# Performance work log

Hardware: AMD Instinct MI355X
Metric: run time of the kernel (lower is better)

## Reference

```python
import jax, jax.numpy as jnp
import numpy as np

I_DIM = 20000        # item (node) count; emb_mat has I_DIM+1 rows
EMB_DIM = 128        # input embedding dim
D_DIM = 128          # hidden (scaled) dim
N_EDGES = 640000     # number of (src, dst) edges


def setup_inputs() -> dict:
    key = jax.random.key(0)
    k1, k2, k3, k4 = jax.random.split(key, 4)
    emb_mat = jax.random.normal(k1, (I_DIM + 1, EMB_DIM), dtype=jnp.float32)
    # edges must be sorted by source node (column 0) so that the original
    # tf.repeat(segment_sums, bincount(src)) trick is well-defined.
    edge = jax.random.randint(k2, (N_EDGES, 2), 0, I_DIM + 1, dtype=jnp.int64)
    order = jnp.argsort(edge[:, 0])
    edge = edge[order]
    W_scale = jax.random.normal(k3, (EMB_DIM, D_DIM), dtype=jnp.float32) * 0.05
    b_scale = jnp.zeros((D_DIM,), dtype=jnp.float32)
    W_att = jax.random.normal(k4, (2 * D_DIM, 1), dtype=jnp.float32) * 0.05
    b_att = jnp.zeros((1,), dtype=jnp.float32)
    return {"emb_mat": emb_mat, "edge": edge, "W_scale": W_scale,
            "b_scale": b_scale, "W_att": W_att, "b_att": b_att}


def reference(emb_mat, edge, W_scale, b_scale, W_att, b_att):
    num_segments = emb_mat.shape[0]          # i_dim + 1
    seg = edge[:, 0]                         # source nodes (segment ids), [E]

    # gather both endpoints, scale: [E, 2, emb] -> [E, 2, d]
    edge_emb = emb_mat[edge] @ W_scale + b_scale
    E = edge_emb.shape[0]
    # attention logit per edge from concatenated endpoint features
    att = (edge_emb.reshape(E, -1) @ W_att + b_att)[:, 0]   # [E]
    att = jax.nn.leaky_relu(att, negative_slope=0.2)
    scores = jnp.exp(att - 1.0)                              # exp(att - ones)

    # manual segment softmax over edges grouped by source node
    score_sum = jax.ops.segment_sum(scores, seg, num_segments=num_segments)
    score_norm = scores / score_sum[seg]                     # [E]

    # scale all node embeddings once, gather destination features
    item_scaled = emb_mat @ W_scale + b_scale                # [N, d]
    items = item_scaled[edge[:, 1]]                          # [E, d]

    agg = jax.ops.segment_sum(score_norm[:, None] * items, seg,
                              num_segments=num_segments)     # [N, d]
    return jax.nn.sigmoid(agg)
```

## Files before the change

### kernel.cpp

```cpp
#include <hip/hip_runtime.h>
#include <math.h>

#define NSEG 20001
#define EMB  128
#define NE   640000

#define SCALE_BLOCKS ((NSEG + 15) / 16)
#define BOUNDS_BLOCKS ((NE + 255) / 256)

__device__ __forceinline__ float dot4(float4 a, float4 b) {
    return a.x*b.x + a.y*b.y + a.z*b.z + a.w*b.w;
}

#define FMA4(acc, s, b) { acc.x += (s)*(b).x; acc.y += (s)*(b).y; acc.z += (s)*(b).z; acc.w += (s)*(b).w; }

__device__ __forceinline__ unsigned short f2bf(float x) {
    unsigned u = __float_as_uint(x);
    unsigned r = (u + 0x7fffu + ((u >> 16) & 1u)) >> 16;
    return (unsigned short)r;
}

__global__ __launch_bounds__(256) void prep_kernel(
    const float* __restrict__ emb, const float* __restrict__ W,
    const float* __restrict__ bsc, const float* __restrict__ Watt,
    const int* __restrict__ edge,
    unsigned short* __restrict__ tab,
    float* __restrict__ a_src, float* __restrict__ a_dst,
    int* __restrict__ seg_start)
{
    const int tid = threadIdx.x;
    if (blockIdx.x >= SCALE_BLOCKS) {
        int e = (blockIdx.x - SCALE_BLOCKS) * 256 + tid;
        if (e >= NE) return;
        int s  = edge[2*e];
        int sp = (e == 0) ? -1 : edge[2*e - 2];
        for (int t = sp + 1; t <= s; ++t) seg_start[t] = e;
        if (e == NE - 1) {
            for (int t = s + 1; t <= NSEG; ++t) seg_start[t] = NE;
        }
        return;
    }

    __shared__ float emb_s[16 * EMB];
    const int r0 = blockIdx.x * 16;

    const float4* embg4 = (const float4*)emb;
    float4* es4 = (float4*)emb_s;
    const int gmax = NSEG * 32 - 1;
    #pragma unroll
    for (int j = 0; j < 2; ++j) {
        int idx = tid + j * 256;
        int g = r0 * 32 + idx;
        es4[idx] = embg4[g <= gmax ? g : gmax];
    }
    __syncthreads();

    const int cg = tid & 31;
    const int rb = (tid >> 5) * 2;

    float4 acc0 = {0.f,0.f,0.f,0.f};
    float4 acc1 = {0.f,0.f,0.f,0.f};
    const float4* Wg4 = (const float4*)W;

    for (int k = 0; k < EMB; k += 4) {
        float4 b0 = Wg4[(k+0)*32 + cg];
        float4 b1 = Wg4[(k+1)*32 + cg];
        float4 b2 = Wg4[(k+2)*32 + cg];
        float4 b3 = Wg4[(k+3)*32 + cg];
        float4 a0 = *(const float4*)&emb_s[(rb+0)*EMB + k];
        float4 a1 = *(const float4*)&emb_s[(rb+1)*EMB + k];
        FMA4(acc0, a0.x, b0); FMA4(acc0, a0.y, b1); FMA4(acc0, a0.z, b2); FMA4(acc0, a0.w, b3);
        FMA4(acc1, a1.x, b0); FMA4(acc1, a1.y, b1); FMA4(acc1, a1.z, b2); FMA4(acc1, a1.w, b3);
    }

    float4 bs = *(const float4*)&bsc[cg*4];
    acc0.x += bs.x; acc0.y += bs.y; acc0.z += bs.z; acc0.w += bs.w;
    acc1.x += bs.x; acc1.y += bs.y; acc1.z += bs.z; acc1.w += bs.w;

    const int row0 = r0 + rb;
    const int row1 = row0 + 1;
    if (row0 < NSEG) {
        ushort4 p = { f2bf(acc0.x), f2bf(acc0.y), f2bf(acc0.z), f2bf(acc0.w) };
        *(ushort4*)&tab[row0*EMB + cg*4] = p;
    }
    if (row1 < NSEG) {
        ushort4 p = { f2bf(acc1.x), f2bf(acc1.y), f2bf(acc1.z), f2bf(acc1.w) };
        *(ushort4*)&tab[row1*EMB + cg*4] = p;
    }

    float4 ws = *(const float4*)&Watt[cg*4];
    float4 wd = *(const float4*)&Watt[EMB + cg*4];
    float p0s = dot4(acc0, ws), p0d = dot4(acc0, wd);
    float p1s = dot4(acc1, ws), p1d = dot4(acc1, wd);
    #pragma unroll
    for (int off = 16; off >= 1; off >>= 1) {
        p0s += __shfl_xor(p0s, off);
        p0d += __shfl_xor(p0d, off);
        p1s += __shfl_xor(p1s, off);
        p1d += __shfl_xor(p1d, off);
    }
    if ((tid & 31) == 0) {
        if (row0 < NSEG) { a_src[row0] = p0s; a_dst[row0] = p0d; }
        if (row1 < NSEG) { a_src[row1] = p1s; a_dst[row1] = p1d; }
    }
}

__device__ __forceinline__ float bcastf(float v, int j) {
    return __uint_as_float(__builtin_amdgcn_readlane(__float_as_uint(v), j));
}
__device__ __forceinline__ float bf_lo(unsigned u) { return __uint_as_float(u << 16); }
__device__ __forceinline__ float bf_hi(unsigned u) { return __uint_as_float(u & 0xffff0000u); }

__global__ __launch_bounds__(256) void agg_kernel(
    const int* __restrict__ edge, const float* __restrict__ a_src,
    const float* __restrict__ a_dst, const float* __restrict__ b_att,
    const int* __restrict__ seg_start, const unsigned int* __restrict__ tab32,
    float* __restrict__ out)
{
    const int wid = blockIdx.x * 4 + (threadIdx.x >> 6);
    if (wid >= NSEG) return;
    const int lane = threadIdx.x & 63;
    const unsigned int* tabl = tab32 + lane;

    const int s0 = seg_start[wid];
    const int s1 = seg_start[wid + 1];
    const float aS = a_src[wid] + b_att[0];

    float accx = 0.f, accy = 0.f, ssum = 0.f;

    for (int cb = s0; cb < s1; cb += 64) {
        int n = s1 - cb; if (n > 64) n = 64;
        int e = cb + lane;
        int dmine = 0; float sc = 0.f;
        if (lane < n) {
            dmine = edge[2*e + 1] << 6;
            float att = aS + a_dst[dmine >> 6];
            att = att > 0.f ? att : 0.2f * att;
            sc  = expf(att - 1.f);
        }
        ssum += sc;

        int j = 0;
        for (; j + 3 < n; j += 4) {
            float w0 = bcastf(sc, j+0), w1 = bcastf(sc, j+1);
            float w2 = bcastf(sc, j+2), w3 = bcastf(sc, j+3);
            int d0 = __builtin_amdgcn_readlane(dmine, j+0);
            int d1 = __builtin_amdgcn_readlane(dmine, j+1);
            int d2 = __builtin_amdgcn_readlane(dmine, j+2);
            int d3 = __builtin_amdgcn_readlane(dmine, j+3);
            unsigned u0 = tabl[d0];
            unsigned u1 = tabl[d1];
            unsigned u2 = tabl[d2];
            unsigned u3 = tabl[d3];
            accx += w0 * bf_lo(u0); accy += w0 * bf_hi(u0);
            accx += w1 * bf_lo(u1); accy += w1 * bf_hi(u1);
            accx += w2 * bf_lo(u2); accy += w2 * bf_hi(u2);
            accx += w3 * bf_lo(u3); accy += w3 * bf_hi(u3);
        }
        for (; j < n; ++j) {
            float w = bcastf(sc, j);
            int   d = __builtin_amdgcn_readlane(dmine, j);
            unsigned u = tabl[d];
            accx += w * bf_lo(u);
            accy += w * bf_hi(u);
        }
    }

    #pragma unroll
    for (int off = 32; off >= 1; off >>= 1) ssum += __shfl_xor(ssum, off);

    const float inv = (s1 > s0) ? 1.f / ssum : 0.f;
    float ox = accx * inv, oy = accy * inv;
    ox = 1.f / (1.f + expf(-ox));
    oy = 1.f / (1.f + expf(-oy));
    *(float2*)&out[wid * EMB + 2 * lane] = make_float2(ox, oy);
}

extern "C" void kernel_launch(void* const* d_in, const int* in_sizes, int n_in,
                              void* d_out, int out_size, void* d_ws, size_t ws_size,
                              hipStream_t stream) {
    const float* emb  = (const float*)d_in[0];
    const int*   edge = (const int*)  d_in[1];
    const float* W    = (const float*)d_in[2];
    const float* bsc  = (const float*)d_in[3];
    const float* Watt = (const float*)d_in[4];
    const float* batt = (const float*)d_in[5];
    float* out = (float*)d_out;

    unsigned short* tab = (unsigned short*)d_ws;
    float* a_src = (float*)(tab + (size_t)NSEG * EMB);
    float* a_dst = a_src + NSEG;
    int*   seg_start = (int*)(a_dst + NSEG);

    prep_kernel<<<SCALE_BLOCKS + BOUNDS_BLOCKS, 256, 0, stream>>>(
        emb, W, bsc, Watt, edge, tab, a_src, a_dst, seg_start);
    agg_kernel<<<(NSEG + 3) / 4, 256, 0, stream>>>(
        edge, a_src, a_dst, batt, seg_start, (const unsigned int*)tab, out);
}
```

Measured before the change: 116.1 us.

## Retile scale GEMM to 64 rows per block and compact destination indices

The prep GEMM now processes 64 rows per block with a padded LDS stride, and each thread computes a 4x8 register tile, reusing W loads across more rows. The bounds pass reads edges as int2, uses a wave shuffle for the previous source id, and writes a compact dst array so the aggregation kernel reads 4 bytes per edge instead of strided pairs. The aggregation inner loop is unrolled to 8 gathers in flight. It costs more registers and LDS per block and an extra workspace write of the destination array.

Result: faster. 111.4 us (-4.1%).

```diff
diff --git a/kernel.cpp b/kernel.cpp
--- a/kernel.cpp
+++ b/kernel.cpp
@@ -5,8 +5,9 @@
 #define EMB  128
 #define NE   640000
 
-#define SCALE_BLOCKS ((NSEG + 15) / 16)
-#define BOUNDS_BLOCKS ((NE + 255) / 256)
+#define SCALE_BLOCKS 313
+#define BOUNDS_BLOCKS 2500
+#define LDSL 129
 
 __device__ __forceinline__ float dot4(float4 a, float4 b) {
     return a.x*b.x + a.y*b.y + a.z*b.z + a.w*b.w;
@@ -14,10 +15,9 @@
 
 #define FMA4(acc, s, b) { acc.x += (s)*(b).x; acc.y += (s)*(b).y; acc.z += (s)*(b).z; acc.w += (s)*(b).w; }
 
-__device__ __forceinline__ unsigned short f2bf(float x) {
+__device__ __forceinline__ unsigned f2bf(float x) {
     unsigned u = __float_as_uint(x);
-    unsigned r = (u + 0x7fffu + ((u >> 16) & 1u)) >> 16;
-    return (unsigned short)r;
+    return (u + 0x7fffu + ((u >> 16) & 1u)) >> 16;
 }
 
 __global__ __launch_bounds__(256) void prep_kernel(
@@ -26,93 +26,101 @@
     const int* __restrict__ edge,
     unsigned short* __restrict__ tab,
     float* __restrict__ a_src, float* __restrict__ a_dst,
-    int* __restrict__ seg_start)
+    int* __restrict__ seg_start, int* __restrict__ dst)
 {
     const int tid = threadIdx.x;
     if (blockIdx.x >= SCALE_BLOCKS) {
         int e = (blockIdx.x - SCALE_BLOCKS) * 256 + tid;
-        if (e >= NE) return;
-        int s  = edge[2*e];
-        int sp = (e == 0) ? -1 : edge[2*e - 2];
-        for (int t = sp + 1; t <= s; ++t) seg_start[t] = e;
+        int2 p = ((const int2*)edge)[e];
+        dst[e] = p.y;
+        int sp = __shfl_up(p.x, 1);
+        if ((tid & 63) == 0) sp = (e == 0) ? -1 : edge[2*e - 2];
+        for (int t = sp + 1; t <= p.x; ++t) seg_start[t] = e;
         if (e == NE - 1) {
-            for (int t = s + 1; t <= NSEG; ++t) seg_start[t] = NE;
+            for (int t = p.x + 1; t <= NSEG; ++t) seg_start[t] = NE;
         }
         return;
     }
 
-    __shared__ float emb_s[16 * EMB];
-    const int r0 = blockIdx.x * 16;
+    __shared__ float emb_s[64 * LDSL];
+    const int r0 = blockIdx.x * 64;
 
     const float4* embg4 = (const float4*)emb;
-    float4* es4 = (float4*)emb_s;
     const int gmax = NSEG * 32 - 1;
     #pragma unroll
-    for (int j = 0; j < 2; ++j) {
+    for (int j = 0; j < 8; ++j) {
         int idx = tid + j * 256;
+        int row = idx >> 5, f4 = idx & 31;
         int g = r0 * 32 + idx;
-        es4[idx] = embg4[g <= gmax ? g : gmax];
+        float4 v = embg4[g <= gmax ? g : gmax];
+        float* p = &emb_s[row * LDSL + f4 * 4];
+        p[0] = v.x; p[1] = v.y; p[2] = v.z; p[3] = v.w;
     }
     __syncthreads();
 
-    const int cg = tid & 31;
-    const int rb = (tid >> 5) * 2;
-
-    float4 acc0 = {0.f,0.f,0.f,0.f};
-    float4 acc1 = {0.f,0.f,0.f,0.f};
+    const int cg   = tid & 15;
+    const int rowb = (tid >> 4) * 4;
+
+    float4 accA[4] = {{0,0,0,0},{0,0,0,0},{0,0,0,0},{0,0,0,0}};
+    float4 accB[4] = {{0,0,0,0},{0,0,0,0},{0,0,0,0},{0,0,0,0}};
     const float4* Wg4 = (const float4*)W;
 
-    for (int k = 0; k < EMB; k += 4) {
-        float4 b0 = Wg4[(k+0)*32 + cg];
-        float4 b1 = Wg4[(k+1)*32 + cg];
-        float4 b2 = Wg4[(k+2)*32 + cg];
-        float4 b3 = Wg4[(k+3)*32 + cg];
-        float4 a0 = *(const float4*)&emb_s[(rb+0)*EMB + k];
-        float4 a1 = *(const float4*)&emb_s[(rb+1)*EMB + k];
-        FMA4(acc0, a0.x, b0); FMA4(acc0, a0.y, b1); FMA4(acc0, a0.z, b2); FMA4(acc0, a0.w, b3);
-        FMA4(acc1, a1.x, b0); FMA4(acc1, a1.y, b1); FMA4(acc1, a1.z, b2); FMA4(acc1, a1.w, b3);
-    }
-
-    float4 bs = *(const float4*)&bsc[cg*4];
-    acc0.x += bs.x; acc0.y += bs.y; acc0.z += bs.z; acc0.w += bs.w;
-    acc1.x += bs.x; acc1.y += bs.y; acc1.z += bs.z; acc1.w += bs.w;
-
-    const int row0 = r0 + rb;
-    const int row1 = row0 + 1;
-    if (row0 < NSEG) {
-        ushort4 p = { f2bf(acc0.x), f2bf(acc0.y), f2bf(acc0.z), f2bf(acc0.w) };
-        *(ushort4*)&tab[row0*EMB + cg*4] = p;
-    }
-    if (row1 < NSEG) {
-        ushort4 p = { f2bf(acc1.x), f2bf(acc1.y), f2bf(acc1.z), f2bf(acc1.w) };
-        *(ushort4*)&tab[row1*EMB + cg*4] = p;
-    }
-
-    float4 ws = *(const float4*)&Watt[cg*4];
-    float4 wd = *(const float4*)&Watt[EMB + cg*4];
-    float p0s = dot4(acc0, ws), p0d = dot4(acc0, wd);
-    float p1s = dot4(acc1, ws), p1d = dot4(acc1, wd);
+    #pragma unroll 4
+    for (int k = 0; k < EMB; ++k) {
+        float4 w0 = Wg4[k*32 + cg*2];
+        float4 w1 = Wg4[k*32 + cg*2 + 1];
+        float a0 = emb_s[(rowb+0)*LDSL + k];
+        float a1 = emb_s[(rowb+1)*LDSL + k];
+        float a2 = emb_s[(rowb+2)*LDSL + k];
+        float a3 = emb_s[(rowb+3)*LDSL + k];
+        FMA4(accA[0], a0, w0); FMA4(accB[0], a0, w1);
+        FMA4(accA[1], a1, w0); FMA4(accB[1], a1, w1);
+        FMA4(accA[2], a2, w0); FMA4(accB[2], a2, w1);
+        FMA4(accA[3], a3, w0); FMA4(accB[3], a3, w1);
+    }
+
+    const float4 bsA = *(const float4*)&bsc[cg*8];
+    const float4 bsB = *(const float4*)&bsc[cg*8 + 4];
+    const float4 wsA = *(const float4*)&Watt[cg*8];
+    const float4 wsB = *(const float4*)&Watt[cg*8 + 4];
+    const float4 wdA = *(const float4*)&Watt[EMB + cg*8];
+    const float4 wdB = *(const float4*)&Watt[EMB + cg*8 + 4];
+
     #pragma unroll
-    for (int off = 16; off >= 1; off >>= 1) {
-        p0s += __shfl_xor(p0s, off);
-        p0d += __shfl_xor(p0d, off);
-        p1s += __shfl_xor(p1s, off);
-        p1d += __shfl_xor(p1d, off);
-    }
-    if ((tid & 31) == 0) {
-        if (row0 < NSEG) { a_src[row0] = p0s; a_dst[row0] = p0d; }
-        if (row1 < NSEG) { a_src[row1] = p1s; a_dst[row1] = p1d; }
-    }
-}
-
+    for (int r = 0; r < 4; ++r) {
+        float4 A = accA[r], B = accB[r];
+        A.x += bsA.x; A.y += bsA.y; A.z += bsA.z; A.w += bsA.w;
+        B.x += bsB.x; B.y += bsB.y; B.z += bsB.z; B.w += bsB.w;
+        const int row = r0 + rowb + r;
+
+        if (row < NSEG) {
+            uint4 pkt;
+            pkt.x = f2bf(A.x) | (f2bf(A.y) << 16);
+            pkt.y = f2bf(A.z) | (f2bf(A.w) << 16);
+            pkt.z = f2bf(B.x) | (f2bf(B.y) << 16);
+            pkt.w = f2bf(B.z) | (f2bf(B.w) << 16);
+            ((uint4*)tab)[row * 16 + cg] = pkt;
+        }
+
+        float ps = dot4(A, wsA) + dot4(B, wsB);
+        float pd = dot4(A, wdA) + dot4(B, wdB);
+        #pragma unroll
+        for (int off = 8; off >= 1; off >>= 1) {
+            ps += __shfl_xor(ps, off);
+            pd += __shfl_xor(pd, off);
+        }
+        if (cg == 0 && row < NSEG) { a_src[row] = ps; a_dst[row] = pd; }
+    }
+}
+
+__device__ __forceinline__ float bf_lo(unsigned u) { return __uint_as_float(u << 16); }
+__device__ __forceinline__ float bf_hi(unsigned u) { return __uint_as_float(u & 0xffff0000u); }
 __device__ __forceinline__ float bcastf(float v, int j) {
     return __uint_as_float(__builtin_amdgcn_readlane(__float_as_uint(v), j));
 }
-__device__ __forceinline__ float bf_lo(unsigned u) { return __uint_as_float(u << 16); }
-__device__ __forceinline__ float bf_hi(unsigned u) { return __uint_as_float(u & 0xffff0000u); }
 
 __global__ __launch_bounds__(256) void agg_kernel(
-    const int* __restrict__ edge, const float* __restrict__ a_src,
+    const int* __restrict__ dst, const float* __restrict__ a_src,
     const float* __restrict__ a_dst, const float* __restrict__ b_att,
     const int* __restrict__ seg_start, const unsigned int* __restrict__ tab32,
     float* __restrict__ out)
@@ -133,7 +141,7 @@
         int e = cb + lane;
         int dmine = 0; float sc = 0.f;
         if (lane < n) {
-            dmine = edge[2*e + 1] << 6;
+            dmine = dst[e] << 6;
             float att = aS + a_dst[dmine >> 6];
             att = att > 0.f ? att : 0.2f * att;
             sc  = expf(att - 1.f);
@@ -141,21 +149,29 @@
         ssum += sc;
 
         int j = 0;
-        for (; j + 3 < n; j += 4) {
+        for (; j + 7 < n; j += 8) {
             float w0 = bcastf(sc, j+0), w1 = bcastf(sc, j+1);
             float w2 = bcastf(sc, j+2), w3 = bcastf(sc, j+3);
+            float w4 = bcastf(sc, j+4), w5 = bcastf(sc, j+5);
+            float w6 = bcastf(sc, j+6), w7 = bcastf(sc, j+7);
             int d0 = __builtin_amdgcn_readlane(dmine, j+0);
             int d1 = __builtin_amdgcn_readlane(dmine, j+1);
             int d2 = __builtin_amdgcn_readlane(dmine, j+2);
             int d3 = __builtin_amdgcn_readlane(dmine, j+3);
-            unsigned u0 = tabl[d0];
-            unsigned u1 = tabl[d1];
-            unsigned u2 = tabl[d2];
-            unsigned u3 = tabl[d3];
+            int d4 = __builtin_amdgcn_readlane(dmine, j+4);
+            int d5 = __builtin_amdgcn_readlane(dmine, j+5);
+            int d6 = __builtin_amdgcn_readlane(dmine, j+6);
+            int d7 = __builtin_amdgcn_readlane(dmine, j+7);
+            unsigned u0 = tabl[d0], u1 = tabl[d1], u2 = tabl[d2], u3 = tabl[d3];
+            unsigned u4 = tabl[d4], u5 = tabl[d5], u6 = tabl[d6], u7 = tabl[d7];
             accx += w0 * bf_lo(u0); accy += w0 * bf_hi(u0);
             accx += w1 * bf_lo(u1); accy += w1 * bf_hi(u1);
             accx += w2 * bf_lo(u2); accy += w2 * bf_hi(u2);
             accx += w3 * bf_lo(u3); accy += w3 * bf_hi(u3);
+            accx += w4 * bf_lo(u4); accy += w4 * bf_hi(u4);
+            accx += w5 * bf_lo(u5); accy += w5 * bf_hi(u5);
+            accx += w6 * bf_lo(u6); accy += w6 * bf_hi(u6);
+            accx += w7 * bf_lo(u7); accy += w7 * bf_hi(u7);
         }
         for (; j < n; ++j) {
             float w = bcastf(sc, j);
@@ -191,9 +207,10 @@
     float* a_src = (float*)(tab + (size_t)NSEG * EMB);
     float* a_dst = a_src + NSEG;
     int*   seg_start = (int*)(a_dst + NSEG);
+    int*   dstc = seg_start + NSEG + 3;
 
     prep_kernel<<<SCALE_BLOCKS + BOUNDS_BLOCKS, 256, 0, stream>>>(
-        emb, W, bsc, Watt, edge, tab, a_src, a_dst, seg_start);
+        emb, W, bsc, Watt, edge, tab, a_src, a_dst, seg_start, dstc);
     agg_kernel<<<(NSEG + 3) / 4, 256, 0, stream>>>(
-        edge, a_src, a_dst, batt, seg_start, (const unsigned int*)tab, out);
-}
+        dstc, a_src, a_dst, batt, seg_start, (const unsigned int*)tab, out);
+}
```
